# Performance work log

Hardware: AMD Instinct MI355X
Metric: run time of the kernel (lower is better)

## Reference

```python
import jax, jax.numpy as jnp
import numpy as np

D_MODEL, D_K, D_V, H, N, B = 512, 64, 64, 8, 2048, 2


def _xavier(key, shape):
    fan_out, fan_in = shape
    a = jnp.sqrt(6.0 / (fan_in + fan_out))
    return jax.random.uniform(key, shape, jnp.float32, -a, a)


def setup_inputs() -> dict:
    key = jax.random.key(0)
    ks = jax.random.split(key, 12)
    inp = {
        "regions_out": jax.random.normal(ks[0], (B, N, D_MODEL), jnp.float32),
        "grids_out": jax.random.normal(ks[1], (B, N, D_MODEL), jnp.float32),
        "interests": jax.random.normal(ks[2], (B, N, D_MODEL), jnp.float32),
        "attention_mask_regions": jax.random.randint(ks[3], (B, 1, 1, N), 0, 2, jnp.int32),
        "attention_mask_grids": jax.random.randint(ks[4], (B, 1, 1, N), 0, 2, jnp.int32),
        "attention_weights": jax.random.uniform(ks[5], (B, 1, 1, N), jnp.float32),
        # nn.Linear params (weight [out,in], bias [out]); xavier_uniform weights, zero bias
        "Wq": _xavier(ks[6], (H * D_K, D_MODEL)), "bq": jnp.zeros((H * D_K,), jnp.float32),
        "Wk": _xavier(ks[7], (H * D_K, D_MODEL)), "bk": jnp.zeros((H * D_K,), jnp.float32),
        "Wv": _xavier(ks[8], (H * D_V, D_MODEL)), "bv": jnp.zeros((H * D_V,), jnp.float32),
        "Wq12": _xavier(ks[9], (H * D_K, D_MODEL)), "bq12": jnp.zeros((H * D_K,), jnp.float32),
        "Wo1": _xavier(ks[10], (D_MODEL, H * D_V)), "bo1": jnp.zeros((D_MODEL,), jnp.float32),
        "Wo2": _xavier(ks[11], (D_MODEL, H * D_V)), "bo2": jnp.zeros((D_MODEL,), jnp.float32),
    }
    return inp


def _proj(x, W, b, d):
    # x: [b, n, d_model] -> [b, h, n, d]
    b_s, n, _ = x.shape
    y = x @ W.T + b
    return y.reshape(b_s, n, H, d).transpose(0, 2, 1, 3)


def reference(regions_out, grids_out, interests, attention_mask_regions,
              attention_mask_grids, attention_weights,
              Wq, bq, Wk, bk, Wv, bv, Wq12, bq12, Wo1, bo1, Wo2, bo2):
    b_s, nq, _ = interests.shape
    scale = 1.0 / np.sqrt(D_K).astype(np.float32)

    q = _proj(interests, Wq, bq, D_K)          # [b,h,nq,dk]
    q1 = _proj(regions_out, Wq12, bq12, D_K)   # [b,h,nk1,dk]
    q2 = _proj(grids_out, Wq12, bq12, D_K)     # [b,h,nk1,dk]
    k1 = _proj(regions_out, Wk, bk, D_K)       # [b,h,nk1,dk]
    k2 = _proj(grids_out, Wk, bk, D_K)
    v1 = _proj(regions_out, Wv, bv, D_V)
    v2 = _proj(grids_out, Wv, bv, D_V)

    att1 = jnp.einsum("bhqd,bhkd->bhqk", q + q2, k1) * scale
    att2 = jnp.einsum("bhqd,bhkd->bhqk", q + q1, k2) * scale
    att1 = att1 * attention_weights
    att2 = att2 * attention_weights
    att1 = jnp.where(attention_mask_regions.astype(bool), -jnp.inf, att1)
    att2 = jnp.where(attention_mask_grids.astype(bool), -jnp.inf, att2)
    att1 = jax.nn.softmax(att1, axis=-1)
    att2 = jax.nn.softmax(att2, axis=-1)
    # dropout is identity in eval mode

    out1 = jnp.einsum("bhqk,bhkd->bhqd", att1, v1).transpose(0, 2, 1, 3).reshape(b_s, nq, H * D_V)
    out2 = jnp.einsum("bhqk,bhkd->bhqd", att2, v2).transpose(0, 2, 1, 3).reshape(b_s, nq, H * D_V)
    out1 = out1 @ Wo1.T + bo1
    out2 = out2 @ Wo2.T + bo2
    return (out1, out2)
```

## Files before the change

kernel.cpp:

```cpp
#include <hip/hip_runtime.h>
#include <hip/hip_bf16.h>

typedef __attribute__((ext_vector_type(8))) __bf16 bf16x8;
typedef __attribute__((ext_vector_type(4))) float f32x4;
typedef __attribute__((ext_vector_type(4))) int   i32x4;
typedef unsigned short u16;

#define WS_SEG 2097152

static __device__ __forceinline__ u16 f2b(float f) {
  __hip_bfloat16 h = __float2bfloat16(f);
  return __builtin_bit_cast(u16, h);
}
static __device__ __forceinline__ i32x4 cvt8(const float* __restrict__ p) {
  float4 a = *(const float4*)p;
  float4 b = *(const float4*)(p + 4);
  union { i32x4 v; u16 u[8]; } r;
  r.u[0]=f2b(a.x); r.u[1]=f2b(a.y); r.u[2]=f2b(a.z); r.u[3]=f2b(a.w);
  r.u[4]=f2b(b.x); r.u[5]=f2b(b.y); r.u[6]=f2b(b.z); r.u[7]=f2b(b.w);
  return r.v;
}
static __device__ __forceinline__ float fexp2(float x) {
  float r; asm("v_exp_f32 %0, %1" : "=v"(r) : "v"(x)); return r;
}
template<int C>
static __device__ __forceinline__ float dppf(float x) {
  int v = __builtin_amdgcn_update_dpp(__builtin_bit_cast(int, x),
                                      __builtin_bit_cast(int, x), C, 0xF, 0xF, false);
  return __builtin_bit_cast(float, v);
}
static __device__ __forceinline__ float rowsum16(float x) {
  x += dppf<0xB1>(x);
  x += dppf<0x4E>(x);
  x += dppf<0x141>(x);
  x += dppf<0x140>(x);
  return x;
}
static __device__ __forceinline__ void gld16(const u16* gp, u16* lp) {
  __builtin_amdgcn_global_load_lds(
      (const __attribute__((address_space(1))) void*)gp,
      (__attribute__((address_space(3))) void*)lp, 16, 0, 0);
}

__global__ __launch_bounds__(256) void convert_kernel(
    const float* __restrict__ regions, const float* __restrict__ grids,
    const float* __restrict__ interests,
    const float* __restrict__ Wq, const float* __restrict__ Wk,
    const float* __restrict__ Wv, const float* __restrict__ Wq12,
    const float* __restrict__ Wo1, const float* __restrict__ Wo2,
    u16* __restrict__ ws)
{
  const size_t i = (size_t)(blockIdx.x * 256 + threadIdx.x) * 8;
  const float* s; u16* d;
  if (i < 2097152)      { s = regions   + i;           d = ws + 6 * WS_SEG + i; }
  else if (i < 4194304) { s = grids     + (i - 2097152); d = ws + 7 * WS_SEG + (i - 2097152); }
  else if (i < 6291456) { s = interests + (i - 4194304); d = ws + 8 * WS_SEG + (i - 4194304); }
  else {
    const size_t j = i - 6291456;
    d = ws + 9 * WS_SEG + j;
    if (j < 262144)       s = Wq  + j;
    else if (j < 524288)  s = Wk  + (j - 262144);
    else if (j < 786432)  s = Wv  + (j - 524288);
    else if (j < 1048576) s = Wq12+ (j - 786432);
    else if (j < 1310720) s = Wo1 + (j - 1048576);
    else                  s = Wo2 + (j - 1310720);
  }
  *(i32x4*)d = cvt8(s);
}

template<int MT, int NM>
__global__ __launch_bounds__(256, 2) void gemm_all(
    const float* __restrict__ aw,
    const float* __restrict__ bq,  const float* __restrict__ bk,
    const float* __restrict__ bv,  const float* __restrict__ bq12,
    const float* __restrict__ bo1, const float* __restrict__ bo2,
    u16* __restrict__ ws, float* __restrict__ out, int phase)
{
  constexpr int MFR = MT / 32;
  __shared__ u16 SM[(MT + 128) * 64];
  u16* As = SM;
  u16* Bs = SM + MT * 64;

  const u16* regs_bf = ws + 6 * WS_SEG;
  const u16* grid_bf = ws + 7 * WS_SEG;
  const u16* intr_bf = ws + 8 * WS_SEG;
  const u16* Wt      = ws + 9 * WS_SEG;

  const int id = blockIdx.x;
  const int m_idx = id % NM;
  const int rest  = id / NM;
  const int j_idx = rest & 3;
  const int z     = rest >> 2;

  const u16 *A1 = nullptr, *A2 = nullptr, *B1 = nullptr, *B2 = nullptr;
  const float *bias1 = nullptr, *bias2 = nullptr;
  u16* dst16 = nullptr;
  float* dst32 = nullptr;
  int KT = 512, epi = 0;
  if (phase == 0) {
    if (z == 0)      { A1=intr_bf; A2=grid_bf; B1=Wt; B2=Wt+786432; KT=1024; bias1=bq; bias2=bq12; epi=0; dst16=ws+0*WS_SEG; }
    else if (z == 1) { A1=intr_bf; A2=regs_bf; B1=Wt; B2=Wt+786432; KT=1024; bias1=bq; bias2=bq12; epi=0; dst16=ws+1*WS_SEG; }
    else if (z == 2) { A1=regs_bf; B1=Wt+262144; bias1=bk; epi=1; dst16=ws+2*WS_SEG; }
    else if (z == 3) { A1=grid_bf; B1=Wt+262144; bias1=bk; epi=1; dst16=ws+3*WS_SEG; }
    else if (z == 4) { A1=regs_bf; B1=Wt+524288; bias1=bv; epi=3; dst16=ws+4*WS_SEG; }
    else             { A1=grid_bf; B1=Wt+524288; bias1=bv; epi=3; dst16=ws+5*WS_SEG; }
  } else {
    if (z == 0) { A1=ws+6*WS_SEG; B1=Wt+1048576; bias1=bo1; epi=2; dst32=out; }
    else        { A1=ws+7*WS_SEG; B1=Wt+1310720; bias1=bo2; epi=2; dst32=out + 2097152; }
  }
  const bool swp = (epi == 3);

  const int t = threadIdx.x;
  const int lane = t & 63, w = t >> 6;
  const int l15 = lane & 15, q4 = lane >> 4;
  const int m0 = m_idx * MT, j0 = j_idx * 128;
  const int ro = (w >> 1) * (MT / 2), co = (w & 1) * 64;

  f32x4 acc[MFR][4];
  for (int i = 0; i < MFR; i++)
    for (int j = 0; j < 4; j++) acc[i][j] = (f32x4){0.f, 0.f, 0.f, 0.f};

  for (int k0 = 0; k0 < KT; k0 += 64) {
    const u16* pa; const u16* pb; int kk = k0, ra, rb;
    if (swp)           { pa = B1; pb = A1; ra = j0; rb = m0; }
    else if (kk < 512) { pa = A1; pb = B1; ra = m0; rb = j0; }
    else               { pa = A2; pb = B2; ra = m0; rb = j0; kk -= 512; }
    __syncthreads();
#pragma unroll
    for (int c = 0; c < MFR; c++) {
      const int cidx = w * MFR + c;
      const int row = cidx * 8 + (lane >> 3);
      const int cg = (lane & 7) ^ (row & 7);
      gld16(&pa[(size_t)(ra + row) * 512 + kk + cg * 8], &As[cidx * 512]);
    }
#pragma unroll
    for (int c = 0; c < 4; c++) {
      const int cidx = w * 4 + c;
      const int row = cidx * 8 + (lane >> 3);
      const int cg = (lane & 7) ^ (row & 7);
      gld16(&pb[(size_t)(rb + row) * 512 + kk + cg * 8], &Bs[cidx * 512]);
    }
    __syncthreads();
#pragma unroll
    for (int h = 0; h < 2; h++) {
      bf16x8 af[MFR], bfr[4];
#pragma unroll
      for (int i = 0; i < MFR; i++) {
        const int r = ro + i * 16 + l15;
        af[i] = *(const bf16x8*)&As[r * 64 + (((h * 4 + q4) ^ (r & 7)) * 8)];
      }
#pragma unroll
      for (int i = 0; i < 4; i++) {
        const int r = co + i * 16 + l15;
        bfr[i] = *(const bf16x8*)&Bs[r * 64 + (((h * 4 + q4) ^ (r & 7)) * 8)];
      }
#pragma unroll
      for (int mt = 0; mt < MFR; mt++)
#pragma unroll
        for (int nt = 0; nt < 4; nt++)
          acc[mt][nt] = __builtin_amdgcn_mfma_f32_16x16x32_bf16(af[mt], bfr[nt], acc[mt][nt], 0, 0, 0);
    }
  }

  if (epi == 2) {
#pragma unroll
    for (int nt = 0; nt < 4; nt++) {
      const int j = j0 + co + nt * 16 + l15;
      const float bsum = bias1[j];
#pragma unroll
      for (int mt = 0; mt < MFR; mt++)
#pragma unroll
        for (int r = 0; r < 4; r++) {
          const int m = m0 + ro + mt * 16 + q4 * 4 + r;
          dst32[m * 512 + j] = acc[mt][nt][r] + bsum;
        }
    }
    return;
  }

  __syncthreads();
  u16* Es = SM + w * (MT / 2) * 64;

  if (epi == 3) {
#pragma unroll
    for (int mt = 0; mt < MFR; mt++)
#pragma unroll
      for (int r = 0; r < 4; r++) {
        const int rr = mt * 16 + q4 * 4 + r;
        const float bias = bias1[j0 + ro + rr];
#pragma unroll
        for (int nt = 0; nt < 4; nt++)
          Es[rr * 64 + (((nt * 2 + (l15 >> 3)) ^ (rr & 7)) * 8) + (l15 & 7)] =
              f2b(acc[mt][nt][r] + bias);
      }
  } else {
    float bsum4[4];
#pragma unroll
    for (int nt = 0; nt < 4; nt++) {
      const int j = j0 + co + nt * 16 + l15;
      bsum4[nt] = bias1[j] + (bias2 ? bias2[j] : 0.f);
    }
#pragma unroll
    for (int mt = 0; mt < MFR; mt++)
#pragma unroll
      for (int r = 0; r < 4; r++) {
        const int rr = mt * 16 + q4 * 4 + r;
        const float awm = (epi == 1) ? 0.18033688f * aw[m0 + ro + rr] : 1.f;
#pragma unroll
        for (int nt = 0; nt < 4; nt++)
          Es[rr * 64 + (((nt * 2 + (l15 >> 3)) ^ (rr & 7)) * 8) + (l15 & 7)] =
              f2b((acc[mt][nt][r] + bsum4[nt]) * awm);
      }
  }
  asm volatile("s_waitcnt lgkmcnt(0)" ::: "memory");

#pragma unroll
  for (int g = 0; g < MT / 16; g++) {
    const int rr2 = g * 8 + (lane >> 3);
    i32x4 val = *(const i32x4*)&Es[rr2 * 64 + (((lane & 7) ^ (rr2 & 7)) * 8)];
    if (epi == 3) {
      const int hd = j0 + ro + rr2;
      const int token0 = m0 + co;
      *(i32x4*)&dst16[((size_t)(token0 >> 11) * 512 + hd) * 2048 + (token0 & 2047) + (lane & 7) * 8] = val;
    } else {
      const int token = m0 + ro + rr2;
      const int bb = token >> 11, nn = token & 2047;
      const int h = (j0 + co) >> 6;
      *(i32x4*)&dst16[((size_t)(bb * 8 + h) * 2048 + nn) * 64 + (lane & 7) * 8] = val;
    }
  }
}

__global__ __launch_bounds__(256, 2) void attn_kernel(
    const int* __restrict__ mask_r, const int* __restrict__ mask_g,
    u16* __restrict__ ws)
{
  const int id = blockIdx.x;
  const int bhf = id & 31;
  const int qt = id >> 5;
  const int path = bhf >> 4, bh = bhf & 15;
  const int b = bh >> 3, h = bh & 7;
  const u16* Q  = (path ? ws + 1 * WS_SEG : ws + 0 * WS_SEG) + (size_t)bh * (2048 * 64) + qt * 128 * 64;
  const u16* K  = (path ? ws + 3 * WS_SEG : ws + 2 * WS_SEG) + (size_t)bh * (2048 * 64);
  const u16* Vg = (path ? ws + 5 * WS_SEG : ws + 4 * WS_SEG) + (size_t)(b * 512 + h * 64) * 2048;
  const int* mask = (path ? mask_g : mask_r) + b * 2048;
  u16* O = (path ? ws + 7 * WS_SEG : ws + 6 * WS_SEG) + (size_t)(b * 2048 + qt * 128) * 512 + h * 64;

  __shared__ u16 Ks[64 * 64];
  __shared__ u16 Vs[64 * 64];
  __shared__ u16 Ps[128 * 64];
  __shared__ float Ms[2048];

  const int t = threadIdx.x, lane = t & 63, w = t >> 6;
  const int l15 = lane & 15, q4 = lane >> 4;

  {
    const int4 a = *(const int4*)&mask[t * 8];
    const int4 c = *(const int4*)&mask[t * 8 + 4];
    float4 f1, f2v;
    f1.x = (a.x ? -1e30f : 0.f) - 16.f; f1.y = (a.y ? -1e30f : 0.f) - 16.f;
    f1.z = (a.z ? -1e30f : 0.f) - 16.f; f1.w = (a.w ? -1e30f : 0.f) - 16.f;
    f2v.x = (c.x ? -1e30f : 0.f) - 16.f; f2v.y = (c.y ? -1e30f : 0.f) - 16.f;
    f2v.z = (c.z ? -1e30f : 0.f) - 16.f; f2v.w = (c.w ? -1e30f : 0.f) - 16.f;
    *(float4*)&Ms[t * 8] = f1;
    *(float4*)&Ms[t * 8 + 4] = f2v;
  }

  bf16x8 qf[2][2];
#pragma unroll
  for (int mt = 0; mt < 2; mt++) {
    const int qrow = w * 32 + mt * 16 + l15;
    qf[mt][0] = *(const bf16x8*)&Q[qrow * 64 + q4 * 8];
    qf[mt][1] = *(const bf16x8*)&Q[qrow * 64 + 32 + q4 * 8];
  }

  float l_run[2][4];
  f32x4 o_acc[2][4];
#pragma unroll
  for (int mt = 0; mt < 2; mt++) {
#pragma unroll
    for (int r = 0; r < 4; r++) l_run[mt][r] = 0.f;
#pragma unroll
    for (int d = 0; d < 4; d++) o_acc[mt][d] = (f32x4){0.f, 0.f, 0.f, 0.f};
  }

  for (int kt = 0; kt < 32; kt++) {
    __syncthreads();
#pragma unroll
    for (int c = 0; c < 2; c++) {
      const int cidx = w * 2 + c;
      const int row = cidx * 8 + (lane >> 3);
      const int cg = (lane & 7) ^ (row & 7);
      gld16(&K[(size_t)(kt * 64 + row) * 64 + cg * 8], &Ks[cidx * 512]);
      gld16(&Vg[(size_t)row * 2048 + kt * 64 + cg * 8], &Vs[cidx * 512]);
    }
    __syncthreads();

    f32x4 s[2][4];
#pragma unroll
    for (int mt = 0; mt < 2; mt++)
#pragma unroll
      for (int nt = 0; nt < 4; nt++) s[mt][nt] = (f32x4){0.f, 0.f, 0.f, 0.f};
#pragma unroll
    for (int nt = 0; nt < 4; nt++)
#pragma unroll
      for (int ss = 0; ss < 2; ss++) {
        const int r = nt * 16 + l15;
        bf16x8 kf = *(const bf16x8*)&Ks[r * 64 + (((ss * 4 + q4) ^ (r & 7)) * 8)];
        s[0][nt] = __builtin_amdgcn_mfma_f32_16x16x32_bf16(qf[0][ss], kf, s[0][nt], 0, 0, 0);
        s[1][nt] = __builtin_amdgcn_mfma_f32_16x16x32_bf16(qf[1][ss], kf, s[1][nt], 0, 0, 0);
      }

#pragma unroll
    for (int nt = 0; nt < 4; nt++) {
      const float bias = Ms[kt * 64 + nt * 16 + l15];
#pragma unroll
      for (int mt = 0; mt < 2; mt++)
#pragma unroll
        for (int r = 0; r < 4; r++) {
          const float p = fexp2(s[mt][nt][r] + bias);
          s[mt][nt][r] = p;
          l_run[mt][r] += p;
        }
    }

#pragma unroll
    for (int mt = 0; mt < 2; mt++)
#pragma unroll
      for (int nt = 0; nt < 4; nt++) {
        const int cg = 2 * nt + (l15 >> 3);
#pragma unroll
        for (int r = 0; r < 4; r++) {
          const int row = w * 32 + mt * 16 + q4 * 4 + r;
          Ps[row * 64 + ((cg ^ (row & 7)) * 8) + (l15 & 7)] = f2b(s[mt][nt][r]);
        }
      }
    asm volatile("s_waitcnt lgkmcnt(0)" ::: "memory");

#pragma unroll
    for (int ss = 0; ss < 2; ss++) {
      bf16x8 pf[2];
#pragma unroll
      for (int mt = 0; mt < 2; mt++) {
        const int row = w * 32 + mt * 16 + l15;
        const int cg = (4 * ss + q4) ^ (row & 7);
        pf[mt] = *(const bf16x8*)&Ps[row * 64 + cg * 8];
      }
#pragma unroll
      for (int dt = 0; dt < 4; dt++) {
        const int r = dt * 16 + l15;
        bf16x8 vf = *(const bf16x8*)&Vs[r * 64 + (((ss * 4 + q4) ^ (r & 7)) * 8)];
        o_acc[0][dt] = __builtin_amdgcn_mfma_f32_16x16x32_bf16(pf[0], vf, o_acc[0][dt], 0, 0, 0);
        o_acc[1][dt] = __builtin_amdgcn_mfma_f32_16x16x32_bf16(pf[1], vf, o_acc[1][dt], 0, 0, 0);
      }
    }
  }

#pragma unroll
  for (int mt = 0; mt < 2; mt++)
#pragma unroll
    for (int r = 0; r < 4; r++) {
      const float inv = 1.f / rowsum16(l_run[mt][r]);
#pragma unroll
      for (int dt = 0; dt < 4; dt++) {
        O[(w * 32 + mt * 16 + q4 * 4 + r) * 512 + dt * 16 + l15] = f2b(o_acc[mt][dt][r] * inv);
      }
    }
}

extern "C" void kernel_launch(void* const* d_in, const int* in_sizes, int n_in,
                              void* d_out, int out_size, void* d_ws, size_t ws_size,
                              hipStream_t stream) {
  const float* regions   = (const float*)d_in[0];
  const float* grids     = (const float*)d_in[1];
  const float* interests = (const float*)d_in[2];
  const int*   mask_r    = (const int*)d_in[3];
  const int*   mask_g    = (const int*)d_in[4];
  const float* aw        = (const float*)d_in[5];
  const float* Wq  = (const float*)d_in[6];  const float* bq  = (const float*)d_in[7];
  const float* Wk  = (const float*)d_in[8];  const float* bk  = (const float*)d_in[9];
  const float* Wv  = (const float*)d_in[10]; const float* bv  = (const float*)d_in[11];
  const float* Wq12= (const float*)d_in[12]; const float* bq12= (const float*)d_in[13];
  const float* Wo1 = (const float*)d_in[14]; const float* bo1 = (const float*)d_in[15];
  const float* Wo2 = (const float*)d_in[16]; const float* bo2 = (const float*)d_in[17];
  u16*   ws  = (u16*)d_ws;
  float* out = (float*)d_out;

  convert_kernel<<<3840, 256, 0, stream>>>(regions, grids, interests,
      Wq, Wk, Wv, Wq12, Wo1, Wo2, ws);
  gemm_all<128, 32><<<768, 256, 0, stream>>>(aw, bq, bk, bv, bq12, bo1, bo2,
      ws, out, 0);
  attn_kernel<<<512, 256, 0, stream>>>(mask_r, mask_g, ws);
  gemm_all<64, 64><<<512, 256, 0, stream>>>(aw, bq, bk, bv, bq12, bo1, bo2,
      ws, out, 1);
}
```

Before: 194.5 us.

## Compact unmasked keys via prefix scan and skip masked K/V work

Adds a scan kernel that builds, per batch and path, a list of unmasked key indices and their count. The K and V projections gather only those rows and skip tiles beyond the count. Attention then loops only over the compacted key tiles, using a bound check in place of the mask table. This removes projection and attention work for masked keys, which the random masks make about half of all keys. The cost is an extra small launch, gathered global loads and a dependence on the mask density.

```diff
diff --git a/kernel.cpp b/kernel.cpp
--- a/kernel.cpp
+++ b/kernel.cpp
@@ -7,6 +7,7 @@
 typedef unsigned short u16;
 
 #define WS_SEG 2097152
+#define TAIL_OFF (9 * WS_SEG + 1572864)
 
 static __device__ __forceinline__ u16 f2b(float f) {
   __hip_bfloat16 h = __float2bfloat16(f);
@@ -40,6 +41,42 @@
   __builtin_amdgcn_global_load_lds(
       (const __attribute__((address_space(1))) void*)gp,
       (__attribute__((address_space(3))) void*)lp, 16, 0, 0);
+}
+
+__global__ __launch_bounds__(256) void scan_kernel(
+    const int* __restrict__ mask_r, const int* __restrict__ mask_g,
+    u16* __restrict__ ws)
+{
+  const int pb = blockIdx.x;
+  const int path = pb >> 1, b = pb & 1;
+  const int* mask = (path ? mask_g : mask_r) + b * 2048;
+  int* base = (int*)(ws + TAIL_OFF);
+  int* idx = base + pb * 2048;
+  int* NcArr = base + 4 * 2048;
+
+  __shared__ int sc[256];
+  const int t = threadIdx.x;
+  int m[8];
+#pragma unroll
+  for (int j = 0; j < 8; j++) m[j] = mask[t * 8 + j];
+  int cnt = 0;
+#pragma unroll
+  for (int j = 0; j < 8; j++) cnt += (m[j] == 0);
+  sc[t] = cnt;
+  __syncthreads();
+  for (int d = 1; d < 256; d <<= 1) {
+    int v = (t >= d) ? sc[t - d] : 0;
+    __syncthreads();
+    sc[t] += v;
+    __syncthreads();
+  }
+  int off = sc[t] - cnt;
+  const int Nc = sc[255];
+#pragma unroll
+  for (int j = 0; j < 8; j++)
+    if (m[j] == 0) idx[off++] = t * 8 + j;
+  for (int j = Nc + t; j < 2048; j += 256) idx[j] = 0;
+  if (t == 0) NcArr[pb] = Nc;
 }
 
 __global__ __launch_bounds__(256) void convert_kernel(
@@ -110,35 +147,63 @@
   }
   const bool swp = (epi == 3);
 
+  int Nc = 1 << 30, mloc = 0, bb = 0;
+  const int* gidx = nullptr;
+  if (phase == 0 && z >= 2) {
+    const int path = (z == 3 || z == 5) ? 1 : 0;
+    bb = m_idx >> 4;
+    const int* base = (const int*)(ws + TAIL_OFF);
+    gidx = base + (path * 2 + bb) * 2048;
+    Nc = base[4 * 2048 + path * 2 + bb];
+    mloc = (m_idx & 15) * 128;
+    if (mloc >= ((Nc + 127) & ~127)) return;
+  }
+
   const int t = threadIdx.x;
   const int lane = t & 63, w = t >> 6;
   const int l15 = lane & 15, q4 = lane >> 4;
-  const int m0 = m_idx * MT, j0 = j_idx * 128;
+  const int m0 = (gidx ? mloc : m_idx * MT), j0 = j_idx * 128;
   const int ro = (w >> 1) * (MT / 2), co = (w & 1) * 64;
+
+  int arows[MFR], brows[4];
+#pragma unroll
+  for (int c = 0; c < MFR; c++) {
+    const int row = (w * MFR + c) * 8 + (lane >> 3);
+    if (swp)            arows[c] = j0 + row;
+    else if (gidx)      arows[c] = bb * 2048 + gidx[m0 + row];
+    else                arows[c] = m0 + row;
+  }
+#pragma unroll
+  for (int c = 0; c < 4; c++) {
+    const int row = (w * 4 + c) * 8 + (lane >> 3);
+    if (!swp)           brows[c] = j0 + row;
+    else if (gidx)      brows[c] = bb * 2048 + gidx[m0 + row];
+    else                brows[c] = m0 + row;
+  }
 
   f32x4 acc[MFR][4];
   for (int i = 0; i < MFR; i++)
     for (int j = 0; j < 4; j++) acc[i][j] = (f32x4){0.f, 0.f, 0.f, 0.f};
 
   for (int k0 = 0; k0 < KT; k0 += 64) {
-    const u16* pa; const u16* pb; int kk = k0, ra, rb;
-    if (swp)           { pa = B1; pb = A1; ra = j0; rb = m0; }
-    else if (kk < 512) { pa = A1; pb = B1; ra = m0; rb = j0; }
-    else               { pa = A2; pb = B2; ra = m0; rb = j0; kk -= 512; }
+    const u16* pa; const u16* pb; int kk = k0;
+    if (swp)           { pa = B1; pb = A1; }
+    else if (kk < 512) { pa = A1; pb = B1; }
+    else               { pa = A2; pb = B2; kk -= 512; }
     __syncthreads();
 #pragma unroll
     for (int c = 0; c < MFR; c++) {
       const int cidx = w * MFR + c;
       const int row = cidx * 8 + (lane >> 3);
       const int cg = (lane & 7) ^ (row & 7);
-      gld16(&pa[(size_t)(ra + row) * 512 + kk + cg * 8], &As[cidx * 512]);
+      gld16(&pa[(size_t)arows[c] * 512 + kk + cg * 8], &As[cidx * 512]);
     }
 #pragma unroll
     for (int c = 0; c < 4; c++) {
       const int cidx = w * 4 + c;
       const int row = cidx * 8 + (lane >> 3);
       const int cg = (lane & 7) ^ (row & 7);
-      gld16(&pb[(size_t)(rb + row) * 512 + kk + cg * 8], &Bs[cidx * 512]);
+      gld16(&pb[(size_t)brows[c] * 512 + kk + cg * 8], &Bs[cidx * 512]);
     }
     __syncthreads();
 #pragma unroll
@@ -189,9 +254,12 @@
         const int rr = mt * 16 + q4 * 4 + r;
         const float bias = bias1[j0 + ro + rr];
 #pragma unroll
-        for (int nt = 0; nt < 4; nt++)
+        for (int nt = 0; nt < 4; nt++) {
+          const int col = m0 + co + nt * 16 + l15;
+          const float v = acc[mt][nt][r] + bias;
           Es[rr * 64 + (((nt * 2 + (l15 >> 3)) ^ (rr & 7)) * 8) + (l15 & 7)] =
-              f2b(acc[mt][nt][r] + bias);
+              (col < Nc) ? f2b(v) : (u16)0;
+        }
       }
   } else {
     float bsum4[4];
@@ -205,11 +273,15 @@
 #pragma unroll
       for (int r = 0; r < 4; r++) {
         const int rr = mt * 16 + q4 * 4 + r;
-        const float awm = (epi == 1) ? 0.18033688f * aw[m0 + ro + rr] : 1.f;
-#pragma unroll
-        for (int nt = 0; nt < 4; nt++)
+        const int i = m0 + ro + rr;
+        float awm = 1.f;
+        if (epi == 1) awm = 0.18033688f * aw[bb * 2048 + gidx[i]];
+#pragma unroll
+        for (int nt = 0; nt < 4; nt++) {
+          const float v = (acc[mt][nt][r] + bsum4[nt]) * awm;
           Es[rr * 64 + (((nt * 2 + (l15 >> 3)) ^ (rr & 7)) * 8) + (l15 & 7)] =
-              f2b((acc[mt][nt][r] + bsum4[nt]) * awm);
+              (i < Nc) ? f2b(v) : (u16)0;
+        }
       }
   }
   asm volatile("s_waitcnt lgkmcnt(0)" ::: "memory");
@@ -220,20 +292,22 @@
     i32x4 val = *(const i32x4*)&Es[rr2 * 64 + (((lane & 7) ^ (rr2 & 7)) * 8)];
     if (epi == 3) {
       const int hd = j0 + ro + rr2;
-      const int token0 = m0 + co;
-      *(i32x4*)&dst16[((size_t)(token0 >> 11) * 512 + hd) * 2048 + (token0 & 2047) + (lane & 7) * 8] = val;
+      const int tok0 = m0 + co;
+      *(i32x4*)&dst16[((size_t)(bb * 512) + hd) * 2048 + tok0 + (lane & 7) * 8] = val;
+    } else if (epi == 1) {
+      const int i = m0 + ro + rr2;
+      const int hh = (j0 + co) >> 6;
+      *(i32x4*)&dst16[((size_t)(bb * 8 + hh) * 2048 + i) * 64 + (lane & 7) * 8] = val;
     } else {
       const int token = m0 + ro + rr2;
-      const int bb = token >> 11, nn = token & 2047;
-      const int h = (j0 + co) >> 6;
-      *(i32x4*)&dst16[((size_t)(bb * 8 + h) * 2048 + nn) * 64 + (lane & 7) * 8] = val;
-    }
-  }
-}
-
-__global__ __launch_bounds__(256, 2) void attn_kernel(
-    const int* __restrict__ mask_r, const int* __restrict__ mask_g,
-    u16* __restrict__ ws)
+      const int b2 = token >> 11, nn = token & 2047;
+      const int hh = (j0 + co) >> 6;
+      *(i32x4*)&dst16[((size_t)(b2 * 8 + hh) * 2048 + nn) * 64 + (lane & 7) * 8] = val;
+    }
+  }
+}
+
+__global__ __launch_bounds__(256, 2) void attn_kernel(u16* __restrict__ ws)
 {
   const int id = blockIdx.x;
   const int bhf = id & 31;
@@ -243,28 +317,18 @@
   const u16* Q  = (path ? ws + 1 * WS_SEG : ws + 0 * WS_SEG) + (size_t)bh * (2048 * 64) + qt * 128 * 64;
   const u16* K  = (path ? ws + 3 * WS_SEG : ws + 2 * WS_SEG) + (size_t)bh * (2048 * 64);
   const u16* Vg = (path ? ws + 5 * WS_SEG : ws + 4 * WS_SEG) + (size_t)(b * 512 + h * 64) * 2048;
-  const int* mask = (path ? mask_g : mask_r) + b * 2048;
   u16* O = (path ? ws + 7 * WS_SEG : ws + 6 * WS_SEG) + (size_t)(b * 2048 + qt * 128) * 512 + h * 64;
+
+  const int* base = (const int*)(ws + TAIL_OFF);
+  const int Nc = base[4 * 2048 + path * 2 + b];
+  const int ktm = (Nc + 63) >> 6;
 
   __shared__ u16 Ks[64 * 64];
   __shared__ u16 Vs[64 * 64];
   __shared__ u16 Ps[128 * 64];
-  __shared__ float Ms[2048];
 
   const int t = threadIdx.x, lane = t & 63, w = t >> 6;
   const int l15 = lane & 15, q4 = lane >> 4;
-
-  {
-    const int4 a = *(const int4*)&mask[t * 8];
-    const int4 c = *(const int4*)&mask[t * 8 + 4];
-    float4 f1, f2v;
-    f1.x = (a.x ? -1e30f : 0.f) - 16.f; f1.y = (a.y ? -1e30f : 0.f) - 16.f;
-    f1.z = (a.z ? -1e30f : 0.f) - 16.f; f1.w = (a.w ? -1e30f : 0.f) - 16.f;
-    f2v.x = (c.x ? -1e30f : 0.f) - 16.f; f2v.y = (c.y ? -1e30f : 0.f) - 16.f;
-    f2v.z = (c.z ? -1e30f : 0.f) - 16.f; f2v.w = (c.w ? -1e30f : 0.f) - 16.f;
-    *(float4*)&Ms[t * 8] = f1;
-    *(float4*)&Ms[t * 8 + 4] = f2v;
-  }
 
   bf16x8 qf[2][2];
 #pragma unroll
@@ -284,7 +348,7 @@
     for (int d = 0; d < 4; d++) o_acc[mt][d] = (f32x4){0.f, 0.f, 0.f, 0.f};
   }
 
-  for (int kt = 0; kt < 32; kt++) {
+  for (int kt = 0; kt < ktm; kt++) {
     __syncthreads();
 #pragma unroll
     for (int c = 0; c < 2; c++) {
@@ -313,7 +377,8 @@
 
 #pragma unroll
     for (int nt = 0; nt < 4; nt++) {
-      const float bias = Ms[kt * 64 + nt * 16 + l15];
+      const int kg = kt * 64 + nt * 16 + l15;
+      const float bias = (kg < Nc) ? -16.f : -1e30f;
 #pragma unroll
       for (int mt = 0; mt < 2; mt++)
 #pragma unroll
@@ -386,11 +451,12 @@
   u16*   ws  = (u16*)d_ws;
   float* out = (float*)d_out;
 
+  scan_kernel<<<4, 256, 0, stream>>>(mask_r, mask_g, ws);
   convert_kernel<<<3840, 256, 0, stream>>>(regions, grids, interests,
       Wq, Wk, Wv, Wq12, Wo1, Wo2, ws);
   gemm_all<128, 32><<<768, 256, 0, stream>>>(aw, bq, bk, bv, bq12, bo1, bo2,
       ws, out, 0);
-  attn_kernel<<<512, 256, 0, stream>>>(mask_r, mask_g, ws);
+  attn_kernel<<<512, 256, 0, stream>>>(ws);
   gemm_all<64, 64><<<512, 256, 0, stream>>>(aw, bq, bk, bv, bq12, bo1, bo2,
       ws, out, 1);
 }
```

New measurement: 176.3 us. -9.4%, faster.
